# Kernel optimization log

Hardware: AMD Instinct MI355X
Metric: run time of the kernel (lower is better)

The kernel has to match this reference:

```python
import jax, jax.numpy as jnp
import numpy as np
import math

D_MODEL = 1024
N_HEAD = 16
D_HEAD = D_MODEL // N_HEAD
SCALE = math.sqrt(D_HEAD)
B, S = 8, 512


def setup_inputs() -> dict:
    key = jax.random.key(0)
    ks = jax.random.split(key, 7)
    x = jax.random.normal(ks[0], (B, S, D_MODEL), dtype=jnp.float32)
    mask = jnp.ones((B, S), dtype=jnp.int32)
    qmask = jax.random.randint(ks[1], (B, S), 0, 2).astype(jnp.int32)
    # params
    Wqkv = jax.random.normal(ks[2], (4 * D_MODEL, D_MODEL), dtype=jnp.float32) / math.sqrt(D_MODEL)
    fc_w = jax.random.normal(ks[3], (D_MODEL, D_MODEL), dtype=jnp.float32) / math.sqrt(D_MODEL)
    fc_b = jnp.zeros((D_MODEL,), dtype=jnp.float32)
    shift = jnp.abs(jax.random.normal(ks[4], (1,), dtype=jnp.float32)) + 0.001
    bias = -jnp.abs(jax.random.normal(ks[5], (1,), dtype=jnp.float32))
    return {"x": x, "mask": mask, "qmask": qmask, "Wqkv": Wqkv,
            "fc_w": fc_w, "fc_b": fc_b, "shift": shift, "bias": bias}


def reference(x, mask, qmask, Wqkv, fc_w, fc_b, shift, bias):
    Bsz, L, D = x.shape
    qkv = x @ Wqkv.T  # [B,S,4D], no bias
    q, k1, k2, v = jnp.split(qkv, 4, axis=-1)

    def heads(t):  # [B,S,D] -> [B,H,S,dh]
        return t.reshape(Bsz, L, N_HEAD, D_HEAD).transpose(0, 2, 1, 3)

    q, k1, k2, v = heads(q), heads(k1), heads(k2), heads(v)

    attn_self = jnp.einsum('bhqd,bhkd->bhqk', q, k1)
    attn_others = jnp.einsum('bhqd,bhkd->bhqk', q, k2)
    same_spk = (qmask[:, :, None] == qmask[:, None, :])[:, None]  # [B,1,S,S]
    attn = jnp.where(same_spk, attn_self, attn_others) / SCALE

    # key padding mask
    attn = jnp.where((mask == 0)[:, None, None, :], -jnp.inf, attn)

    # Gaussian distance bias: -(shift*(i-j)^2 + bias)
    pos = jnp.arange(L, dtype=jnp.float32)
    sq_dist = (pos[:, None] - pos[None, :]) ** 2  # [S,S]
    attn = attn - (shift[0] * sq_dist + bias[0])

    p = jax.nn.softmax(attn, axis=-1)  # dropout=0 (eval)
    out = jnp.einsum('bhqk,bhkd->bhqd', p, v)
    out = out.transpose(0, 2, 1, 3).reshape(Bsz, L, D)
    return out @ fc_w.T + fc_b
```

## Files before the change

kernel.cpp:

```cpp
#include <hip/hip_runtime.h>

typedef unsigned short u16;
typedef __bf16 bf16_t;
typedef bf16_t bf16x8 __attribute__((ext_vector_type(8)));
typedef float f32x4 __attribute__((ext_vector_type(4)));
typedef u16 u16x8 __attribute__((ext_vector_type(8)));
typedef u16 u16x4 __attribute__((ext_vector_type(4)));

__device__ __forceinline__ u16 f2b(float f) {
    unsigned int u = __float_as_uint(f);
    u += 0x7fffu + ((u >> 16) & 1u);
    return (u16)(u >> 16);
}

__device__ __forceinline__ f32x4 mfma16(u16x8 a, u16x8 b, f32x4 c) {
    return __builtin_amdgcn_mfma_f32_16x16x32_bf16(
        __builtin_bit_cast(bf16x8, a), __builtin_bit_cast(bf16x8, b), c, 0, 0, 0);
}

#define GLDS16(gp, lp)                                                          \
    __builtin_amdgcn_global_load_lds(                                           \
        (const __attribute__((address_space(1))) void*)(gp),                    \
        (__attribute__((address_space(3))) void*)(lp), 16, 0, 0)

__global__ __launch_bounds__(256) void cvt3_kernel(const float* __restrict__ s0,
                                                   const float* __restrict__ s1,
                                                   const float* __restrict__ s2,
                                                   u16* __restrict__ d0,
                                                   u16* __restrict__ d1,
                                                   u16* __restrict__ d2) {
    int i = (blockIdx.x * 256 + threadIdx.x) * 4;
    const float* src; u16* dst;
    if (i < 4194304)       { src = s0;           dst = d0;           }
    else if (i < 8388608)  { src = s1 - 4194304; dst = d1 - 4194304; }
    else                   { src = s2 - 8388608; dst = d2 - 8388608; }
    float4 f = *(const float4*)(src + i);
    u16x4 o = { f2b(f.x), f2b(f.y), f2b(f.z), f2b(f.w) };
    *(u16x4*)(dst + i) = o;
}

template <int MT, int MODE>
__global__ __launch_bounds__(256) void gemm_bt(
    const u16* __restrict__ A, const u16* __restrict__ Bw,
    u16* __restrict__ Qf, u16* __restrict__ K1f,
    u16* __restrict__ K2f, u16* __restrict__ Vf,
    float* __restrict__ Cf, const float* __restrict__ biasp)
{
    constexpr int K = 1024;
    constexpr int MF = MT / 32;
    __shared__ u16 As[2][MT * 32];
    __shared__ u16 Bs[2][128 * 32];
    const int t = threadIdx.x;
    const int lane = t & 63;
    const int w = t >> 6;
    const int wm = w >> 1, wn = w & 1;
    const int lr = lane & 15, quad = lane >> 4;
    const int tileM = blockIdx.y * MT, tileN = blockIdx.x * 128;

    f32x4 acc[MF][4] = {};

    const u16* Ag = A + (size_t)(tileM + (t >> 2)) * K + (t & 3) * 8;
    const u16* Bg = Bw + (size_t)(tileN + (t >> 2)) * K + (t & 3) * 8;

#define STAGE(kk, bufi)                                                         \
    do {                                                                        \
        GLDS16(Ag + (kk), &As[bufi][t * 8]);                                    \
        if (MT == 128) GLDS16(Ag + (kk) + 64 * K, &As[bufi][t * 8 + 2048]);     \
        GLDS16(Bg + (kk), &Bs[bufi][t * 8]);                                    \
        GLDS16(Bg + (kk) + 64 * K, &Bs[bufi][t * 8 + 2048]);                    \
    } while (0)

    STAGE(0, 0);
    __syncthreads();

#pragma unroll 2
    for (int kk = 0; kk < K; kk += 32) {
        const int cur = (kk >> 5) & 1;
        if (kk + 32 < K) STAGE(kk + 32, cur ^ 1);

        u16x8 af[MF], bf[4];
#pragma unroll
        for (int i = 0; i < MF; ++i)
            af[i] = *(const u16x8*)(&As[cur][(wm * (MT / 2) + i * 16 + lr) * 32 + quad * 8]);
#pragma unroll
        for (int i = 0; i < 4; ++i)
            bf[i] = *(const u16x8*)(&Bs[cur][(wn * 64 + i * 16 + lr) * 32 + quad * 8]);
#pragma unroll
        for (int mi = 0; mi < MF; ++mi)
#pragma unroll
            for (int ni = 0; ni < 4; ++ni)
                acc[mi][ni] = mfma16(af[mi], bf[ni], acc[mi][ni]);

        __syncthreads();
    }
#undef STAGE

    if (MODE == 0) {
#pragma unroll
        for (int mi = 0; mi < MF; ++mi)
#pragma unroll
            for (int ni = 0; ni < 4; ++ni) {
                int n = tileN + wn * 64 + ni * 16 + lr;
                int kv = n >> 10;
                int h = (n >> 6) & 15, d = n & 63;
#pragma unroll
                for (int r = 0; r < 4; ++r) {
                    int m = tileM + wm * (MT / 2) + mi * 16 + quad * 4 + r;
                    int s = m & 511, bh = ((m >> 9) << 4) + h;
                    u16 v = f2b(acc[mi][ni][r]);
                    if (kv < 3) {
                        u16* base = (kv == 0) ? Qf : (kv == 1) ? K1f : K2f;
                        size_t idx = ((size_t)((bh * 32 + (s >> 4)) * 2 + (d >> 5))) * 512
                                   + (((d >> 3) & 3) * 16 + (s & 15)) * 8 + (d & 7);
                        base[idx] = v;
                    } else {
                        size_t idx = ((size_t)((bh * 4 + (d >> 4)) * 16 + (s >> 5))) * 512
                                   + (((s >> 3) & 3) * 16 + (d & 15)) * 8 + (s & 7);
                        Vf[idx] = v;
                    }
                }
            }
    } else {
#pragma unroll
        for (int mi = 0; mi < MF; ++mi)
#pragma unroll
            for (int ni = 0; ni < 4; ++ni) {
                int n = tileN + wn * 64 + ni * 16 + lr;
                float bv = biasp[n];
#pragma unroll
                for (int r = 0; r < 4; ++r) {
                    int m = tileM + wm * (MT / 2) + mi * 16 + quad * 4 + r;
                    Cf[(size_t)m * 1024 + n] = acc[mi][ni][r] + bv;
                }
            }
    }
}

__global__ __launch_bounds__(256) void attn_kernel(
    const u16* __restrict__ qfm, const u16* __restrict__ k1fm,
    const u16* __restrict__ k2fm, const u16* __restrict__ vfm,
    const int* __restrict__ maskp, const int* __restrict__ qmaskp,
    const float* __restrict__ shiftp, const float* __restrict__ biasp,
    u16* __restrict__ ao)
{
    __shared__ u16 Ks[2][2][2][2][512];
    __shared__ u16 Vs[2][4][512];
    __shared__ u16 Pw[4][512];

    const int bh = blockIdx.x & 127, qt = blockIdx.x >> 7;
    const int b = bh >> 4;
    const int t = threadIdx.x, lane = t & 63, w = t >> 6;
    const int lr = lane & 15, quad = lane >> 4;
    const float shiftv = shiftp[0], biasv = biasp[0];

    const int m16 = qt * 4 + w;
    const int qbase = m16 * 16;

    const u16* qsrc = qfm + ((size_t)(bh * 32 + m16) * 2) * 512 + lane * 8;
    u16x8 qa0 = *(const u16x8*)(qsrc);
    u16x8 qa1 = *(const u16x8*)(qsrc + 512);

    int qmr[4]; float rowf[4];
#pragma unroll
    for (int r = 0; r < 4; ++r) {
        int m = qbase + quad * 4 + r;
        qmr[r] = qmaskp[b * 512 + m];
        rowf[r] = (float)m;
    }

    f32x4 o0 = {0.f,0.f,0.f,0.f}, o1 = {0.f,0.f,0.f,0.f};
    f32x4 o2 = {0.f,0.f,0.f,0.f}, o3 = {0.f,0.f,0.f,0.f};
    float lsum[4] = {0.f, 0.f, 0.f, 0.f};

    u16* pbuf = &Pw[w][0];
    const int wa0 = quad * 128 + (((lr >> 3) ^ quad) * 8) + (lr & 7);
    const int wa1 = quad * 128 + (((2 | (lr >> 3)) ^ quad) * 8) + (lr & 7);
    const int ra = lr * 32 + ((quad ^ (lr >> 2)) * 8);

    const int s_ = w >> 1, kh_ = w & 1;
    const u16* k1s = k1fm + ((size_t)(bh * 32 + s_) * 2 + kh_) * 512 + lane * 8;
    const u16* k2s = k2fm + ((size_t)(bh * 32 + s_) * 2 + kh_) * 512 + lane * 8;
    const u16* vsrc = vfm + ((size_t)(bh * 4 + w) * 16) * 512 + lane * 8;

#define ASTAGE(cc, bufi)                                                        \
    do {                                                                        \
        GLDS16(k1s + (size_t)(cc) * 2048, &Ks[bufi][0][s_][kh_][lane * 8]);     \
        GLDS16(k2s + (size_t)(cc) * 2048, &Ks[bufi][1][s_][kh_][lane * 8]);     \
        GLDS16(vsrc + (size_t)(cc) * 512, &Vs[bufi][w][lane * 8]);              \
    } while (0)

    const int* qmb = qmaskp + b * 512;
    const int* kmb = maskp + b * 512;

    ASTAGE(0, 0);
    __syncthreads();

    for (int cc = 0; cc < 16; ++cc) {
        const int cur = cc & 1;
        if (cc < 15) ASTAGE(cc + 1, cur ^ 1);

        u16x8 k1t0a = *(const u16x8*)(&Ks[cur][0][0][0][lane * 8]);
        u16x8 k1t0b = *(const u16x8*)(&Ks[cur][0][0][1][lane * 8]);
        u16x8 k1t1a = *(const u16x8*)(&Ks[cur][0][1][0][lane * 8]);
        u16x8 k1t1b = *(const u16x8*)(&Ks[cur][0][1][1][lane * 8]);
        u16x8 k2t0a = *(const u16x8*)(&Ks[cur][1][0][0][lane * 8]);
        u16x8 k2t0b = *(const u16x8*)(&Ks[cur][1][0][1][lane * 8]);
        u16x8 k2t1a = *(const u16x8*)(&Ks[cur][1][1][0][lane * 8]);
        u16x8 k2t1b = *(const u16x8*)(&Ks[cur][1][1][1][lane * 8]);

        f32x4 z = {0.f, 0.f, 0.f, 0.f};
        f32x4 s1t0 = mfma16(qa1, k1t0b, mfma16(qa0, k1t0a, z));
        f32x4 s2t0 = mfma16(qa1, k2t0b, mfma16(qa0, k2t0a, z));
        f32x4 s1t1 = mfma16(qa1, k1t1b, mfma16(qa0, k1t1a, z));
        f32x4 s2t1 = mfma16(qa1, k2t1b, mfma16(qa0, k2t1a, z));

        const int col0 = cc * 32 + lr, col1 = col0 + 16;
        const int qmc0 = qmb[col0], qmc1 = qmb[col1];
        const float ka0 = (kmb[col0] ? 0.f : -1e30f) - 10.0f;
        const float ka1 = (kmb[col1] ? 0.f : -1e30f) - 10.0f;
        const float colf0 = (float)col0, colf1 = (float)col1;

        float p0[4], p1[4];
#pragma unroll
        for (int r = 0; r < 4; ++r) {
            float d0 = rowf[r] - colf0;
            float d1 = rowf[r] - colf1;
            float sel0 = (qmr[r] == qmc0) ? s1t0[r] : s2t0[r];
            float sel1 = (qmr[r] == qmc1) ? s1t1[r] : s2t1[r];
            float v0 = fmaf(sel0, 0.125f, -fmaf(shiftv * d0, d0, biasv)) + ka0;
            float v1 = fmaf(sel1, 0.125f, -fmaf(shiftv * d1, d1, biasv)) + ka1;
            p0[r] = __expf(v0);
            p1[r] = __expf(v1);
            lsum[r] += p0[r] + p1[r];
        }
#pragma unroll
        for (int r = 0; r < 4; ++r) {
            pbuf[wa0 + r * 32] = f2b(p0[r]);
            pbuf[wa1 + r * 32] = f2b(p1[r]);
        }
        u16x8 af = *(const u16x8*)(pbuf + ra);

        o0 = mfma16(af, *(const u16x8*)(&Vs[cur][0][lane * 8]), o0);
        o1 = mfma16(af, *(const u16x8*)(&Vs[cur][1][lane * 8]), o1);
        o2 = mfma16(af, *(const u16x8*)(&Vs[cur][2][lane * 8]), o2);
        o3 = mfma16(af, *(const u16x8*)(&Vs[cur][3][lane * 8]), o3);

        __syncthreads();
    }
#undef ASTAGE

#pragma unroll
    for (int r = 0; r < 4; ++r) {
        float s = lsum[r];
#pragma unroll
        for (int m = 1; m < 16; m <<= 1) s += __shfl_xor(s, m);
        float inv = 1.0f / s;
        int grow = b * 512 + qbase + quad * 4 + r;
        u16* orow = ao + (size_t)grow * 1024 + (bh & 15) * 64 + lr;
        orow[0]  = f2b(o0[r] * inv);
        orow[16] = f2b(o1[r] * inv);
        orow[32] = f2b(o2[r] * inv);
        orow[48] = f2b(o3[r] * inv);
    }
}

extern "C" void kernel_launch(void* const* d_in, const int* in_sizes, int n_in,
                              void* d_out, int out_size, void* d_ws, size_t ws_size,
                              hipStream_t stream) {
    (void)in_sizes; (void)n_in; (void)out_size; (void)ws_size;
    const float* x      = (const float*)d_in[0];
    const int*   maskp  = (const int*)d_in[1];
    const int*   qmaskp = (const int*)d_in[2];
    const float* Wqkv   = (const float*)d_in[3];
    const float* fc_w   = (const float*)d_in[4];
    const float* fc_b   = (const float*)d_in[5];
    const float* shiftp = (const float*)d_in[6];
    const float* biasp  = (const float*)d_in[7];
    float* out = (float*)d_out;

    char* ws = (char*)d_ws;
    u16* xb   = (u16*)(ws);
    u16* wb   = (u16*)(ws + (8u << 20));
    u16* fwb  = (u16*)(ws + (16u << 20));
    u16* qfm  = (u16*)(ws + (18u << 20));
    u16* k1fm = (u16*)(ws + (26u << 20));
    u16* k2fm = (u16*)(ws + (34u << 20));
    u16* vfm  = (u16*)(ws + (42u << 20));
    u16* aob  = (u16*)(ws + (50u << 20));

    cvt3_kernel<<<9216, 256, 0, stream>>>(x, Wqkv, fc_w, xb, wb, fwb);
    gemm_bt<128, 0><<<dim3(32, 32), 256, 0, stream>>>(xb, wb, qfm, k1fm, k2fm, vfm,
                                                      nullptr, nullptr);
    attn_kernel<<<1024, 256, 0, stream>>>(qfm, k1fm, k2fm, vfm, maskp, qmaskp,
                                          shiftp, biasp, aob);
    gemm_bt<64, 1><<<dim3(8, 64), 256, 0, stream>>>(aob, fwb, nullptr, nullptr,
                                                    nullptr, nullptr, out, fc_b);
}
```

Measured before the change: 204.1 us.

## Replace QKV GEMM with 256x256-tile, 4-stage pipelined 512-thread kernel

Adds a dedicated QKV projection GEMM that uses 256x256 output tiles with 8 waves, a 4-buffer LDS ring filled by direct global-to-LDS loads, XOR-swizzled LDS layout, and block-index swizzling for L2 locality. Per-wave MFMA work is split into two halves interleaved with staging, and setprio is raised around MFMA bursts. The goal is more data reuse per tile and better overlap of memory and compute than the 128x128 double-buffered kernel. The epilogue writes the same fragment-major Q/K1/K2/V layouts. In exchange it uses 128KB of LDS and heavy register pressure, and the 256-block grid may leave some CUs idle.

Result: faster. 183.5 us (-10.1%).

```diff
diff --git a/kernel.cpp b/kernel.cpp
--- a/kernel.cpp
+++ b/kernel.cpp
@@ -37,6 +37,130 @@
     float4 f = *(const float4*)(src + i);
     u16x4 o = { f2b(f.x), f2b(f.y), f2b(f.z), f2b(f.w) };
     *(u16x4*)(dst + i) = o;
+}
+
+__global__ __launch_bounds__(512, 2) void gemm256_qkv(
+    const u16* __restrict__ A, const u16* __restrict__ Bw,
+    u16* __restrict__ Qf, u16* __restrict__ K1f,
+    u16* __restrict__ K2f, u16* __restrict__ Vf)
+{
+    __shared__ u16 lds[4][2][8192];
+
+    const int t = threadIdx.x;
+    const int lane = t & 63;
+    const int w = t >> 6;
+    const int wm = w >> 2, wn = w & 3;
+    const int lr = lane & 15, quad = lane >> 4;
+
+    const int lin = blockIdx.x;
+    const int swz = (lin & 7) * 32 + (lin >> 3);
+    const int bx = swz & 15, by = swz >> 4;
+    const int tileM = by * 256, tileN = bx * 256;
+
+    const int srow = t >> 2;
+    const int scol = ((t & 3) ^ ((t >> 3) & 3)) * 8;
+    const u16* Asrc0 = A + (size_t)(tileM + srow) * 1024 + scol;
+    const u16* Asrc1 = Asrc0 + (size_t)128 * 1024;
+    const u16* Bsrc0 = Bw + (size_t)(tileN + srow) * 1024 + scol;
+    const u16* Bsrc1 = Bsrc0 + (size_t)128 * 1024;
+
+    const int swzq = (quad ^ ((lr >> 1) & 3)) * 8;
+    const int aoff = (wm * 128 + lr) * 32 + swzq;
+    const int boff = (wn * 64 + lr) * 32 + swzq;
+
+    f32x4 acc[8][4] = {};
+
+#define STAGE_A(tk, buf)                                                        \
+    do { GLDS16(Asrc0 + (tk) * 32, &lds[buf][0][t * 8]);                        \
+         GLDS16(Asrc1 + (tk) * 32, &lds[buf][0][(t + 512) * 8]); } while (0)
+#define STAGE_B(tk, buf)                                                        \
+    do { GLDS16(Bsrc0 + (tk) * 32, &lds[buf][1][t * 8]);                        \
+         GLDS16(Bsrc1 + (tk) * 32, &lds[buf][1][(t + 512) * 8]); } while (0)
+
+    STAGE_A(0, 0); STAGE_B(0, 0);
+    STAGE_A(1, 1); STAGE_B(1, 1);
+    STAGE_A(2, 2); STAGE_B(2, 2);
+    asm volatile("s_waitcnt vmcnt(8)" ::: "memory");
+    __builtin_amdgcn_s_barrier();
+
+#pragma unroll 4
+    for (int tk = 0; tk < 32; ++tk) {
+        const int cur = tk & 3;
+        const int nxt = (tk + 3) & 3;
+        const u16* aL = &lds[cur][0][0];
+        const u16* bL = &lds[cur][1][0];
+        const bool st = (tk < 29);
+
+        u16x8 af[4], bf[4];
+
+#pragma unroll
+        for (int i = 0; i < 4; ++i) af[i] = *(const u16x8*)(aL + aoff + i * 512);
+#pragma unroll
+        for (int i = 0; i < 4; ++i) bf[i] = *(const u16x8*)(bL + boff + i * 512);
+        if (st) STAGE_A(tk + 3, nxt);
+        __builtin_amdgcn_s_barrier();
+        asm volatile("s_waitcnt lgkmcnt(0)" ::: "memory");
+        __builtin_amdgcn_sched_barrier(0);
+        __builtin_amdgcn_s_setprio(1);
+#pragma unroll
+        for (int mi = 0; mi < 4; ++mi)
+#pragma unroll
+            for (int ni = 0; ni < 4; ++ni)
+                acc[mi][ni] = mfma16(af[mi], bf[ni], acc[mi][ni]);
+        __builtin_amdgcn_s_setprio(0);
+        __builtin_amdgcn_s_barrier();
+
+#pragma unroll
+        for (int i = 0; i < 4; ++i) af[i] = *(const u16x8*)(aL + aoff + (i + 4) * 512);
+        if (st) STAGE_B(tk + 3, nxt);
+        if (tk < 29)       asm volatile("s_waitcnt vmcnt(8)" ::: "memory");
+        else if (tk == 29) asm volatile("s_waitcnt vmcnt(4)" ::: "memory");
+        else               asm volatile("s_waitcnt vmcnt(0)" ::: "memory");
+        __builtin_amdgcn_s_barrier();
+        asm volatile("s_waitcnt lgkmcnt(0)" ::: "memory");
+        __builtin_amdgcn_sched_barrier(0);
+        __builtin_amdgcn_s_setprio(1);
+#pragma unroll
+        for (int mi = 0; mi < 4; ++mi)
+#pragma unroll
+            for (int ni = 0; ni < 4; ++ni)
+                acc[mi + 4][ni] = mfma16(af[mi], bf[ni], acc[mi + 4][ni]);
+        __builtin_amdgcn_s_setprio(0);
+        __builtin_amdgcn_s_barrier();
+    }
+#undef STAGE_A
+#undef STAGE_B
+
+    const int kv = tileN >> 10;
+    const int h  = ((tileN + wn * 64) >> 6) & 15;
+    const int bh = (((tileM + wm * 128) >> 9) << 4) + h;
+    const int M16 = ((tileM & 511) + wm * 128) >> 4;
+    const int M32 = M16 >> 1;
+
+    if (kv < 3) {
+        u16* base = (kv == 0) ? Qf : (kv == 1) ? K1f : K2f;
+#pragma unroll
+        for (int mi = 0; mi < 8; ++mi)
+#pragma unroll
+            for (int ni = 0; ni < 4; ++ni) {
+                size_t idx0 = ((size_t)((bh * 32 + M16 + mi) * 2 + (ni >> 1))) * 512
+                            + (((ni * 2 + (lr >> 3)) & 3) * 16 + quad * 4) * 8 + (lr & 7);
+#pragma unroll
+                for (int r = 0; r < 4; ++r)
+                    base[idx0 + r * 8] = f2b(acc[mi][ni][r]);
+            }
+    } else {
+#pragma unroll
+        for (int mi = 0; mi < 8; ++mi)
+#pragma unroll
+            for (int ni = 0; ni < 4; ++ni) {
+                size_t idx = ((size_t)((bh * 4 + ni) * 16 + M32 + (mi >> 1))) * 512
+                           + (((mi * 2 + (quad >> 1)) & 3) * 16 + lr) * 8 + (quad & 1) * 4;
+                u16x4 o = { f2b(acc[mi][ni][0]), f2b(acc[mi][ni][1]),
+                            f2b(acc[mi][ni][2]), f2b(acc[mi][ni][3]) };
+                *(u16x4*)(Vf + idx) = o;
+            }
+    }
 }
 
 template <int MT, int MODE>
@@ -289,8 +413,7 @@
     u16* aob  = (u16*)(ws + (50u << 20));
 
     cvt3_kernel<<<9216, 256, 0, stream>>>(x, Wqkv, fc_w, xb, wb, fwb);
-    gemm_bt<128, 0><<<dim3(32, 32), 256, 0, stream>>>(xb, wb, qfm, k1fm, k2fm, vfm,
-                                                      nullptr, nullptr);
+    gemm256_qkv<<<256, 512, 0, stream>>>(xb, wb, qfm, k1fm, k2fm, vfm);
     attn_kernel<<<1024, 256, 0, stream>>>(qfm, k1fm, k2fm, vfm, maskp, qmaskp,
                                           shiftp, biasp, aob);
     gemm_bt<64, 1><<<dim3(8, 64), 256, 0, stream>>>(aob, fwb, nullptr, nullptr,
```
